# Kernel tuning notes

Measured on AMD Instinct MI355X. Metric: run time of the kernel, lower is better.

The kernel has to match this reference:

```python
import jax, jax.numpy as jnp
import numpy as np

B, T, N, H = 4, 256, 16, 256
NHEAD = 8
FFN = 1024
WIN = 8
EPS = 1e-5


def setup_inputs() -> dict:
    key = jax.random.key(0)
    ks = jax.random.split(key, 10)
    s = 0.02
    return {
        "x": jax.random.normal(ks[0], (B, T, N, H), dtype=jnp.float32),
        "key_padding_mask": jnp.zeros((B, T, N), dtype=bool),
        "Wq": jax.random.normal(ks[1], (H, H), dtype=jnp.float32) * s,
        "bq": jnp.zeros((H,), dtype=jnp.float32),
        "Wk": jax.random.normal(ks[2], (H, H), dtype=jnp.float32) * s,
        "bk": jnp.zeros((H,), dtype=jnp.float32),
        "Wv": jax.random.normal(ks[3], (H, H), dtype=jnp.float32) * s,
        "bv": jnp.zeros((H,), dtype=jnp.float32),
        "W1": jax.random.normal(ks[4], (H, FFN), dtype=jnp.float32) * s,
        "b1": jnp.zeros((FFN,), dtype=jnp.float32),
        "W2": jax.random.normal(ks[5], (FFN, H), dtype=jnp.float32) * s,
        "b2": jnp.zeros((H,), dtype=jnp.float32),
        "g1": jnp.ones((H,), dtype=jnp.float32),
        "beta1": jnp.zeros((H,), dtype=jnp.float32),
        "g2": jnp.ones((H,), dtype=jnp.float32),
        "beta2": jnp.zeros((H,), dtype=jnp.float32),
    }


def _layer_norm(x, g, b):
    m = jnp.mean(x, axis=-1, keepdims=True)
    v = jnp.mean(jnp.square(x - m), axis=-1, keepdims=True)
    return (x - m) * jax.lax.rsqrt(v + EPS) * g + b


def reference(x, key_padding_mask, Wq, bq, Wk, bk, Wv, bv, W1, b1, W2, b2, g1, beta1, g2, beta2):
    Bq, Tq, Nq, Hq = x.shape
    D = Hq // NHEAD
    W = 2 * WIN + 1
    # projections
    q = (x @ Wq + bq).reshape(Bq, Tq, Nq, NHEAD, D) / np.float32(np.sqrt(D))
    k = (x @ Wk + bk).reshape(Bq, Tq, Nq, NHEAD, D)
    v = (x @ Wv + bv).reshape(Bq, Tq, Nq, NHEAD, D)
    idx = jnp.arange(Tq)[:, None] + jnp.arange(W)[None, :] - WIN  # (T, W)
    valid = (idx >= 0) & (idx < Tq)                               # (T, W)
    cidx = jnp.clip(idx, 0, Tq - 1)
    vf6 = valid.reshape(1, Tq, W, 1, 1, 1).astype(q.dtype)
    # gathered window keys/values, zero outside clip: (B, T, W, N, h, D)
    wk = jnp.take(k, cidx, axis=1) * vf6
    wv = jnp.take(v, cidx, axis=1) * vf6
    # attention logits over (W, N) neighbors per head
    logits = jnp.einsum('btnhd,btwmhd->btnwmh', q, wk)  # (B,T,N,W,N,h)
    # mask: padded detections within window, plus out-of-range frames
    kpm_g = jnp.take(key_padding_mask, cidx, axis=1)          # (B,T,W,N)
    mask = jnp.where(valid[None, :, :, None], kpm_g, True)    # (B,T,W,N)
    logits = jnp.where(mask[:, :, None, :, :, None], -jnp.inf, logits)
    attn = jax.nn.softmax(logits.reshape(Bq, Tq, Nq, W * Nq, NHEAD), axis=-2)
    ctx = jnp.einsum('btnmh,btmhd->btnhd', attn,
                     wv.reshape(Bq, Tq, W * Nq, NHEAD, D)).reshape(Bq, Tq, Nq, Hq)
    # residual + LN + FFN + residual + LN (dropout = identity in eval)
    y = _layer_norm(x + ctx, g1, beta1)
    ff = jax.nn.relu(y @ W1 + b1) @ W2 + b2
    return _layer_norm(y + ff, g2, beta2)
```

## Files before the change

kernel.cpp:

```cpp
#include <hip/hip_runtime.h>
#include <hip/hip_bf16.h>
#include <math.h>

typedef __attribute__((ext_vector_type(8))) short short8;
typedef __attribute__((ext_vector_type(4))) float float4v;

#define BB 4
#define TT 256
#define NDET 16
#define HH 256
#define NHEAD 8
#define DD 32
#define FFNDIM 1024
#define ROWS (BB*TT*NDET)
#define EPS 1e-5f

__device__ __forceinline__ unsigned short f2bf(float f) {
  unsigned int u = __float_as_uint(f);
  u += 0x7fffu + ((u >> 16) & 1u);
  return (unsigned short)(u >> 16);
}

__device__ __forceinline__ void wt_tile(const float* __restrict__ W, unsigned short* __restrict__ WT,
                                        int K, int N, int k0, int n0,
                                        float (*tile)[33], int tid) {
  {
    int r = tid >> 3, c4 = (tid & 7) * 4;
    float4 in = *(const float4*)(W + (size_t)(k0 + r) * N + n0 + c4);
    tile[r][c4 + 0] = in.x; tile[r][c4 + 1] = in.y;
    tile[r][c4 + 2] = in.z; tile[r][c4 + 3] = in.w;
  }
  __syncthreads();
  {
    int n = tid >> 3, k4 = (tid & 7) * 4;
    ushort4 o;
    o.x = f2bf(tile[k4 + 0][n]); o.y = f2bf(tile[k4 + 1][n]);
    o.z = f2bf(tile[k4 + 2][n]); o.w = f2bf(tile[k4 + 3][n]);
    *(ushort4*)(WT + (size_t)(n0 + n) * K + k0 + k4) = o;
  }
}

__global__ void prep_kernel(const float* __restrict__ x, const unsigned char* __restrict__ kpm,
                            const float* __restrict__ Wq, const float* __restrict__ Wk,
                            const float* __restrict__ Wv, const float* __restrict__ W1,
                            const float* __restrict__ W2,
                            const float* __restrict__ bq, const float* __restrict__ bk,
                            const float* __restrict__ bv,
                            unsigned short* __restrict__ xb, unsigned short* __restrict__ WqkvT,
                            unsigned short* __restrict__ W1T, unsigned short* __restrict__ W2T,
                            unsigned short* __restrict__ kpm16, float* __restrict__ bqkv) {
  __shared__ float tile[32][33];
  int bid = blockIdx.x, tid = threadIdx.x;
  if (bid < 4096) {
    size_t i = (size_t)(bid * 256 + tid) * 4;
    float4 v = *(const float4*)(x + i);
    ushort4 o = { f2bf(v.x), f2bf(v.y), f2bf(v.z), f2bf(v.w) };
    *(ushort4*)(xb + i) = o;
  } else if (bid < 4288) {
    int t = bid - 4096;
    int wsel = t >> 6, tt = t & 63;
    const float* W = (wsel == 0) ? Wq : (wsel == 1) ? Wk : Wv;
    wt_tile(W, WqkvT + wsel * 65536, 256, 256, (tt >> 3) * 32, (tt & 7) * 32, tile, tid);
  } else if (bid < 4544) {
    int tt = bid - 4288;
    wt_tile(W1, W1T, 256, 1024, (tt >> 5) * 32, (tt & 31) * 32, tile, tid);
  } else if (bid < 4800) {
    int tt = bid - 4544;
    wt_tile(W2, W2T, 1024, 256, (tt >> 3) * 32, (tt & 7) * 32, tile, tid);
  } else if (bid < 4804) {
    int w = (bid - 4800) * 256 + tid;
    uint4 u = *(const uint4*)(kpm + (size_t)w * 16);
    unsigned int a[4] = {u.x, u.y, u.z, u.w};
    unsigned int bits = 0;
#pragma unroll
    for (int m = 0; m < 16; ++m)
      if ((a[m >> 2] >> ((m & 3) * 8)) & 0xffu) bits |= (1u << m);
    kpm16[w] = (unsigned short)bits;
  } else {
    bqkv[tid] = bq[tid];
    bqkv[256 + tid] = bk[tid];
    bqkv[512 + tid] = bv[tid];
  }
}

template<int NROWS, int K>
__device__ __forceinline__ void stage_rows(const unsigned short* __restrict__ src, int kcol0,
                                           char* ldsbase, int tid) {
  constexpr int ISS = NROWS / 32;
  int wave = tid >> 6, lane = tid & 63;
#pragma unroll
  for (int i = 0; i < ISS; ++i) {
    int flat = i * 4096 + wave * 1024 + lane * 16;
    int r = flat >> 7;
    int cb = flat & 127;
    int scb = cb ^ ((r & 7) << 4);
    const unsigned short* g = src + (size_t)r * K + kcol0 + (scb >> 1);
    char* l = ldsbase + i * 4096 + wave * 1024;
    __builtin_amdgcn_global_load_lds((const __attribute__((address_space(1))) void*)g,
                                     (__attribute__((address_space(3))) void*)l, 16, 0, 0);
  }
}

template<int EPI>
__launch_bounds__(256, 2)
__global__ void gemm_kernel(const unsigned short* __restrict__ A,
                            const unsigned short* __restrict__ Bt,
                            const float* __restrict__ bias,
                            unsigned short* __restrict__ q_o, unsigned short* __restrict__ k_o,
                            unsigned short* __restrict__ v_o,
                            unsigned short* __restrict__ outb,
                            const float* __restrict__ yres,
                            const float* __restrict__ gw, const float* __restrict__ bw,
                            float* __restrict__ outf) {
  constexpr int BM = (EPI == 2) ? 64 : 128;
  constexpr int BN = (EPI == 2) ? 256 : 128;
  constexpr int K  = (EPI == 2) ? 1024 : 256;
  constexpr int KP = K / 64;
  constexpr int SMEM = (EPI == 2) ? 67072 : (BM + BN) * 128;
  __shared__ char smem[SMEM];
  const int tid = threadIdx.x;
  const int wave = tid >> 6, lane = tid & 63;
  const int lrow = lane & 15, g = lane >> 4;
  const int m0 = blockIdx.x * BM;
  const int n0 = blockIdx.y * BN;
  const int wr = (EPI == 2) ? 0 : (wave >> 1);
  const int wc = (EPI == 2) ? wave : (wave & 1);
  char* As = smem;
  char* Bs = smem + BM * 128;
  float4v acc[4][4];
#pragma unroll
  for (int i = 0; i < 4; ++i)
#pragma unroll
    for (int j = 0; j < 4; ++j) acc[i][j] = (float4v){0.f, 0.f, 0.f, 0.f};

  const unsigned short* Abase = A + (size_t)m0 * K;
  const unsigned short* Bbase = Bt + (size_t)n0 * K;
  for (int ph = 0; ph < KP; ++ph) {
    if (ph) __syncthreads();
    stage_rows<BM, K>(Abase, ph * 64, As, tid);
    stage_rows<BN, K>(Bbase, ph * 64, Bs, tid);
    __syncthreads();
#pragma unroll
    for (int ks = 0; ks < 2; ++ks) {
      short8 af[4], bf[4];
#pragma unroll
      for (int i = 0; i < 4; ++i) {
        int ar = wr * 64 + i * 16 + lrow;
        af[i] = *(const short8*)(As + ar * 128 + ((ks * 64 + g * 16) ^ ((ar & 7) << 4)));
      }
#pragma unroll
      for (int j = 0; j < 4; ++j) {
        int br = wc * 64 + j * 16 + lrow;
        bf[j] = *(const short8*)(Bs + br * 128 + ((ks * 64 + g * 16) ^ ((br & 7) << 4)));
      }
#pragma unroll
      for (int i = 0; i < 4; ++i)
#pragma unroll
        for (int j = 0; j < 4; ++j)
          acc[i][j] = __builtin_amdgcn_mfma_f32_16x16x32_bf16(af[i], bf[j], acc[i][j], 0, 0, 0);
    }
  }

  if (EPI == 0) {
#pragma unroll
    for (int i = 0; i < 4; ++i)
#pragma unroll
      for (int j = 0; j < 4; ++j) {
        int C = n0 + wc * 64 + j * 16 + lrow;
        float bv = bias[C];
        int proj = C >> 8, cc = C & 255;
        int h = cc >> 5, d = cc & 31;
        unsigned short* om = (proj == 0) ? q_o : ((proj == 1) ? k_o : v_o);
        float sc = (proj == 0) ? 0.17677669529663687f : 1.f;
#pragma unroll
        for (int r = 0; r < 4; ++r) {
          int grow = m0 + wr * 64 + i * 16 + g * 4 + r;
          int b = grow >> 12, tn = grow & 4095;
          om[(size_t)((b * 8 + h) * 4096 + tn) * 32 + d] = f2bf((acc[i][j][r] + bv) * sc);
        }
      }
  } else if (EPI == 1) {
#pragma unroll
    for (int i = 0; i < 4; ++i)
#pragma unroll
      for (int j = 0; j < 4; ++j) {
        int C = n0 + wc * 64 + j * 16 + lrow;
        float bv = bias[C];
#pragma unroll
        for (int r = 0; r < 4; ++r) {
          int grow = m0 + wr * 64 + i * 16 + g * 4 + r;
          outb[(size_t)grow * FFNDIM + C] = f2bf(fmaxf(acc[i][j][r] + bv, 0.f));
        }
      }
  } else {
    __syncthreads();
    float* lnb = (float*)smem;
    float* mrow = (float*)(smem + 64 * 260 * 4);
    float* rrow = mrow + 64;
#pragma unroll
    for (int i = 0; i < 4; ++i)
#pragma unroll
      for (int j = 0; j < 4; ++j) {
        int col = wc * 64 + j * 16 + lrow;
        float bv = bias[col];
#pragma unroll
        for (int r = 0; r < 4; ++r) {
          int ml = i * 16 + g * 4 + r;
          lnb[ml * 260 + col] = acc[i][j][r] + bv + yres[(size_t)(m0 + ml) * 256 + col];
        }
      }
    __syncthreads();
    {
      int row = tid >> 2, part = tid & 3;
      float sm = 0.f;
      for (int ii = 0; ii < 64; ++ii) sm += lnb[row * 260 + part + ii * 4];
      sm += __shfl_xor(sm, 1); sm += __shfl_xor(sm, 2);
      float mean = sm * (1.f / 256.f);
      float vv = 0.f;
      for (int ii = 0; ii < 64; ++ii) {
        float dv = lnb[row * 260 + part + ii * 4] - mean;
        vv += dv * dv;
      }
      vv += __shfl_xor(vv, 1); vv += __shfl_xor(vv, 2);
      if (part == 0) { mrow[row] = mean; rrow[row] = rsqrtf(vv * (1.f / 256.f) + EPS); }
    }
    __syncthreads();
    float gg = gw[tid], bb = bw[tid];
    for (int row = 0; row < 64; ++row) {
      float val = (lnb[row * 260 + tid] - mrow[row]) * rrow[row] * gg + bb;
      outf[(size_t)(m0 + row) * 256 + tid] = val;
    }
  }
}

__global__ void vt_kernel(const unsigned short* __restrict__ v, unsigned short* __restrict__ vT) {
  __shared__ unsigned short tl[64][41];
  int bh = blockIdx.x >> 6, tb = blockIdx.x & 63;
  int tid = threadIdx.x;
  {
    int r = tid >> 2, dp = (tid & 3) * 8;
    short8 in = *(const short8*)(v + ((size_t)bh * 4096 + tb * 64 + r) * 32 + dp);
#pragma unroll
    for (int j = 0; j < 8; ++j) tl[r][dp + j] = (unsigned short)in[j];
  }
  __syncthreads();
  {
    int d = tid >> 3, rp = (tid & 7) * 8;
    short8 ov;
#pragma unroll
    for (int j = 0; j < 8; ++j) ov[j] = (short)tl[rp + j][d];
    *(short8*)(vT + ((size_t)bh * 32 + d) * 4096 + tb * 64 + rp) = ov;
  }
}

__launch_bounds__(64)
__global__ void attn_kernel(const unsigned short* __restrict__ qb,
                            const unsigned short* __restrict__ kb,
                            const unsigned short* __restrict__ vT,
                            const unsigned short* __restrict__ kpm16,
                            float* __restrict__ ctx) {
  __shared__ char P[16 * 640];
  int l = threadIdx.x;
  int idx = blockIdx.x;
  int h = idx & 7, t = (idx >> 3) & 255, b = idx >> 11;
  int lrow = l & 15, g = l >> 4;
  int swz = (lrow & 7) << 4;
#pragma unroll
  for (int i = 0; i < 40; ++i) ((int*)P)[l + i * 64] = 0;
  size_t base = (size_t)(b * 8 + h) * 4096;
  short8 qf = *(const short8*)(qb + (base + t * 16 + lrow) * 32 + g * 8);
  const float4v z4 = {0.f, 0.f, 0.f, 0.f};
  float4v s[17];
#pragma unroll
  for (int w = 0; w < 17; ++w) {
    int j = t + w - 8;
    if (j >= 0 && j < 256) {
      short8 kf = *(const short8*)(kb + (base + j * 16 + lrow) * 32 + g * 8);
      float4v sv = __builtin_amdgcn_mfma_f32_16x16x32_bf16(kf, qf, z4, 0, 0, 0);
      unsigned int mw = kpm16[b * 256 + j];
#pragma unroll
      for (int r = 0; r < 4; ++r)
        if ((mw >> (g * 4 + r)) & 1u) sv[r] = -INFINITY;
      s[w] = sv;
    } else {
      s[w] = (float4v){-INFINITY, -INFINITY, -INFINITY, -INFINITY};
    }
  }
  float mx = -INFINITY;
#pragma unroll
  for (int w = 0; w < 17; ++w)
#pragma unroll
    for (int r = 0; r < 4; ++r) mx = fmaxf(mx, s[w][r]);
  mx = fmaxf(mx, __shfl_xor(mx, 16));
  mx = fmaxf(mx, __shfl_xor(mx, 32));
  float sum = 0.f;
#pragma unroll
  for (int w = 0; w < 17; ++w)
#pragma unroll
    for (int r = 0; r < 4; ++r) {
      float e = __expf(s[w][r] - mx);
      s[w][r] = e; sum += e;
    }
  sum += __shfl_xor(sum, 16);
  sum += __shfl_xor(sum, 32);
  float inv = 1.f / sum;
#pragma unroll
  for (int w = 0; w < 17; ++w) {
#pragma unroll
    for (int r0 = 0; r0 < 4; r0 += 2) {
      unsigned int u = (unsigned int)f2bf(s[w][r0]) | ((unsigned int)f2bf(s[w][r0 + 1]) << 16);
      int kbyte = ((w * 16 + g * 4 + r0) * 2) ^ swz;
      *(int*)(P + lrow * 640 + kbyte) = u;
    }
  }
  __syncthreads();
  float4v o0 = z4, o1 = z4;
  int tn0 = (t - 8) * 16;
  const unsigned short* vbase = vT + ((size_t)(b * 8 + h) * 32 + lrow) * 4096;
#pragma unroll
  for (int c = 0; c < 9; ++c) {
    short8 pf = *(const short8*)(P + lrow * 640 + ((c * 64 + g * 16) ^ swz));
    short8 v0 = *(const short8*)(vbase + tn0 + c * 32 + g * 8);
    short8 v1 = *(const short8*)(vbase + (size_t)16 * 4096 + tn0 + c * 32 + g * 8);
    o0 = __builtin_amdgcn_mfma_f32_16x16x32_bf16(pf, v0, o0, 0, 0, 0);
    o1 = __builtin_amdgcn_mfma_f32_16x16x32_bf16(pf, v1, o1, 0, 0, 0);
  }
  size_t orow = ((size_t)(b * 256 + t)) * 16;
  int col = h * 32 + lrow;
#pragma unroll
  for (int r = 0; r < 4; ++r) {
    float invn = __shfl(inv, g * 4 + r);
    size_t rr = (orow + g * 4 + r) * 256 + col;
    ctx[rr] = o0[r] * invn;
    ctx[rr + 16] = o1[r] * invn;
  }
}

__device__ __forceinline__ float block_sum256(float val, float* sc) {
#pragma unroll
  for (int off = 32; off; off >>= 1) val += __shfl_xor(val, off);
  int wid = threadIdx.x >> 6;
  __syncthreads();
  if ((threadIdx.x & 63) == 0) sc[wid] = val;
  __syncthreads();
  return sc[0] + sc[1] + sc[2] + sc[3];
}

__global__ void ln1_kernel(const float* __restrict__ x, const float* __restrict__ ctxv,
                           const float* __restrict__ gw, const float* __restrict__ bw,
                           float* __restrict__ y, unsigned short* __restrict__ yb) {
  __shared__ float sc[4];
  int row = blockIdx.x, tid = threadIdx.x;
  size_t i = (size_t)row * 256 + tid;
  float val = x[i] + ctxv[i];
  float mean = block_sum256(val, sc) * (1.f / 256.f);
  float dv = val - mean;
  float var = block_sum256(dv * dv, sc) * (1.f / 256.f);
  float o = dv * rsqrtf(var + EPS) * gw[tid] + bw[tid];
  y[i] = o;
  yb[i] = f2bf(o);
}

extern "C" void kernel_launch(void* const* d_in, const int* in_sizes, int n_in,
                              void* d_out, int out_size, void* d_ws, size_t ws_size,
                              hipStream_t stream) {
  const float* x  = (const float*)d_in[0];
  const unsigned char* kpm = (const unsigned char*)d_in[1];
  const float* Wq = (const float*)d_in[2];
  const float* bq = (const float*)d_in[3];
  const float* Wk = (const float*)d_in[4];
  const float* bk = (const float*)d_in[5];
  const float* Wv = (const float*)d_in[6];
  const float* bv = (const float*)d_in[7];
  const float* W1 = (const float*)d_in[8];
  const float* b1 = (const float*)d_in[9];
  const float* W2 = (const float*)d_in[10];
  const float* b2 = (const float*)d_in[11];
  const float* g1 = (const float*)d_in[12];
  const float* be1= (const float*)d_in[13];
  const float* g2 = (const float*)d_in[14];
  const float* be2= (const float*)d_in[15];
  float* out = (float*)d_out;

  char* w = (char*)d_ws;
  const size_t MB = 1u << 20;
  unsigned short* xb   = (unsigned short*)(w);
  unsigned short* qhm  = (unsigned short*)(w + 8 * MB);
  unsigned short* khm  = (unsigned short*)(w + 16 * MB);
  unsigned short* vhm  = (unsigned short*)(w + 24 * MB);
  unsigned short* vTb  = (unsigned short*)(w + 32 * MB);
  float*  ctxv = (float*)(w + 40 * MB);
  float*  yv   = (float*)(w + 56 * MB);
  unsigned short* WqkvT = (unsigned short*)(w + 72 * MB);
  unsigned short* W1T = WqkvT + 196608;
  unsigned short* W2T = W1T + 262144;
  unsigned short* kpm16 = W2T + 262144;
  float* bqkv = (float*)(kpm16 + 1024);
  unsigned short* hid = qhm;
  unsigned short* yb  = xb;

  prep_kernel<<<4805, 256, 0, stream>>>(x, kpm, Wq, Wk, Wv, W1, W2, bq, bk, bv,
                                        xb, WqkvT, W1T, W2T, kpm16, bqkv);
  gemm_kernel<0><<<dim3(128, 6), 256, 0, stream>>>(xb, WqkvT, bqkv, qhm, khm, vhm,
                                                   nullptr, nullptr, nullptr, nullptr, nullptr);
  vt_kernel<<<2048, 256, 0, stream>>>(vhm, vTb);
  attn_kernel<<<8192, 64, 0, stream>>>(qhm, khm, vTb, kpm16, ctxv);
  ln1_kernel<<<16384, 256, 0, stream>>>(x, ctxv, g1, be1, yv, yb);
  gemm_kernel<1><<<dim3(128, 8), 256, 0, stream>>>(yb, W1T, b1, nullptr, nullptr, nullptr,
                                                   hid, nullptr, nullptr, nullptr, nullptr);
  gemm_kernel<2><<<dim3(256, 1), 256, 0, stream>>>(hid, W2T, b2, nullptr, nullptr, nullptr,
                                                   nullptr, yv, g2, be2, out);
}
```

Before: 123.9 us.

## Use bf16 intermediates, 4-head attention blocks, exp2 softmax, new fused FFN2+LN kernel

Several changes land together. The attention context and the LN1 output are now stored as bf16 instead of fp32, and LN1 reads the bf16 copy of x and uses one wave per row with a single-pass mean and variance. Attention packs four heads into each 256-thread block, drops the zeroing of P, uses hardware exp2 with log2e folded into the q scale, and packs bf16 with a single conversion instruction. The FFN2 GEMM with its LayerNorm epilogue moves into a new 512-thread kernel whose row statistics come from register shuffles rather than an LDS pass. Together these cut global memory traffic and instruction count, at the cost of extra bf16 rounding on the residual input and a one-pass variance formula that is less numerically robust.

```diff
diff --git a/kernel.cpp b/kernel.cpp
--- a/kernel.cpp
+++ b/kernel.cpp
@@ -19,6 +19,15 @@
   unsigned int u = __float_as_uint(f);
   u += 0x7fffu + ((u >> 16) & 1u);
   return (unsigned short)(u >> 16);
+}
+__device__ __forceinline__ float bf2f(unsigned short u) {
+  return __uint_as_float((unsigned int)u << 16);
+}
+__device__ __forceinline__ float exp2v(float x) {
+  float r; asm("v_exp_f32 %0, %1" : "=v"(r) : "v"(x)); return r;
+}
+__device__ __forceinline__ unsigned int cvtpk(float lo, float hi) {
+  unsigned int r; asm("v_cvt_pk_bf16_f32 %0, %1, %2" : "=v"(r) : "v"(lo), "v"(hi)); return r;
 }
 
 __device__ __forceinline__ void wt_tile(const float* __restrict__ W, unsigned short* __restrict__ WT,
@@ -83,19 +92,19 @@
   }
 }
 
-template<int NROWS, int K>
+template<int NROWS, int K, int NT>
 __device__ __forceinline__ void stage_rows(const unsigned short* __restrict__ src, int kcol0,
                                            char* ldsbase, int tid) {
-  constexpr int ISS = NROWS / 32;
-  int wave = tid >> 6, lane = tid & 63;
+  constexpr int ISS = NROWS * 8 / NT;
+  int wave = tid >> 6;
 #pragma unroll
   for (int i = 0; i < ISS; ++i) {
-    int flat = i * 4096 + wave * 1024 + lane * 16;
+    int flat = i * (NT * 16) + tid * 16;
     int r = flat >> 7;
     int cb = flat & 127;
     int scb = cb ^ ((r & 7) << 4);
     const unsigned short* g = src + (size_t)r * K + kcol0 + (scb >> 1);
-    char* l = ldsbase + i * 4096 + wave * 1024;
+    char* l = ldsbase + i * (NT * 16) + wave * 1024;
     __builtin_amdgcn_global_load_lds((const __attribute__((address_space(1))) void*)g,
                                      (__attribute__((address_space(3))) void*)l, 16, 0, 0);
   }
@@ -108,23 +117,15 @@
                             const float* __restrict__ bias,
                             unsigned short* __restrict__ q_o, unsigned short* __restrict__ k_o,
                             unsigned short* __restrict__ v_o,
-                            unsigned short* __restrict__ outb,
-                            const float* __restrict__ yres,
-                            const float* __restrict__ gw, const float* __restrict__ bw,
-                            float* __restrict__ outf) {
-  constexpr int BM = (EPI == 2) ? 64 : 128;
-  constexpr int BN = (EPI == 2) ? 256 : 128;
-  constexpr int K  = (EPI == 2) ? 1024 : 256;
-  constexpr int KP = K / 64;
-  constexpr int SMEM = (EPI == 2) ? 67072 : (BM + BN) * 128;
-  __shared__ char smem[SMEM];
+                            unsigned short* __restrict__ outb) {
+  constexpr int BM = 128, BN = 128, K = 256, KP = K / 64;
+  __shared__ char smem[(BM + BN) * 128];
   const int tid = threadIdx.x;
   const int wave = tid >> 6, lane = tid & 63;
   const int lrow = lane & 15, g = lane >> 4;
   const int m0 = blockIdx.x * BM;
   const int n0 = blockIdx.y * BN;
-  const int wr = (EPI == 2) ? 0 : (wave >> 1);
-  const int wc = (EPI == 2) ? wave : (wave & 1);
+  const int wr = wave >> 1, wc = wave & 1;
   char* As = smem;
   char* Bs = smem + BM * 128;
   float4v acc[4][4];
@@ -137,8 +138,8 @@
   const unsigned short* Bbase = Bt + (size_t)n0 * K;
   for (int ph = 0; ph < KP; ++ph) {
     if (ph) __syncthreads();
-    stage_rows<BM, K>(Abase, ph * 64, As, tid);
-    stage_rows<BN, K>(Bbase, ph * 64, Bs, tid);
+    stage_rows<BM, K, 256>(Abase, ph * 64, As, tid);
+    stage_rows<BN, K, 256>(Bbase, ph * 64, Bs, tid);
     __syncthreads();
 #pragma unroll
     for (int ks = 0; ks < 2; ++ks) {
@@ -162,6 +163,7 @@
   }
 
   if (EPI == 0) {
+    const float QS = 0.17677669529663687f * 1.4426950408889634f;
 #pragma unroll
     for (int i = 0; i < 4; ++i)
 #pragma unroll
@@ -171,7 +173,7 @@
         int proj = C >> 8, cc = C & 255;
         int h = cc >> 5, d = cc & 31;
         unsigned short* om = (proj == 0) ? q_o : ((proj == 1) ? k_o : v_o);
-        float sc = (proj == 0) ? 0.17677669529663687f : 1.f;
+        float sc = (proj == 0) ? QS : 1.f;
 #pragma unroll
         for (int r = 0; r < 4; ++r) {
           int grow = m0 + wr * 64 + i * 16 + g * 4 + r;
@@ -179,7 +181,7 @@
           om[(size_t)((b * 8 + h) * 4096 + tn) * 32 + d] = f2bf((acc[i][j][r] + bv) * sc);
         }
       }
-  } else if (EPI == 1) {
+  } else {
 #pragma unroll
     for (int i = 0; i < 4; ++i)
 #pragma unroll
@@ -192,44 +194,6 @@
           outb[(size_t)grow * FFNDIM + C] = f2bf(fmaxf(acc[i][j][r] + bv, 0.f));
         }
       }
-  } else {
-    __syncthreads();
-    float* lnb = (float*)smem;
-    float* mrow = (float*)(smem + 64 * 260 * 4);
-    float* rrow = mrow + 64;
-#pragma unroll
-    for (int i = 0; i < 4; ++i)
-#pragma unroll
-      for (int j = 0; j < 4; ++j) {
-        int col = wc * 64 + j * 16 + lrow;
-        float bv = bias[col];
-#pragma unroll
-        for (int r = 0; r < 4; ++r) {
-          int ml = i * 16 + g * 4 + r;
-          lnb[ml * 260 + col] = acc[i][j][r] + bv + yres[(size_t)(m0 + ml) * 256 + col];
-        }
-      }
-    __syncthreads();
-    {
-      int row = tid >> 2, part = tid & 3;
-      float sm = 0.f;
-      for (int ii = 0; ii < 64; ++ii) sm += lnb[row * 260 + part + ii * 4];
-      sm += __shfl_xor(sm, 1); sm += __shfl_xor(sm, 2);
-      float mean = sm * (1.f / 256.f);
-      float vv = 0.f;
-      for (int ii = 0; ii < 64; ++ii) {
-        float dv = lnb[row * 260 + part + ii * 4] - mean;
-        vv += dv * dv;
-      }
-      vv += __shfl_xor(vv, 1); vv += __shfl_xor(vv, 2);
-      if (part == 0) { mrow[row] = mean; rrow[row] = rsqrtf(vv * (1.f / 256.f) + EPS); }
-    }
-    __syncthreads();
-    float gg = gw[tid], bb = bw[tid];
-    for (int row = 0; row < 64; ++row) {
-      float val = (lnb[row * 260 + tid] - mrow[row]) * rrow[row] * gg + bb;
-      outf[(size_t)(m0 + row) * 256 + tid] = val;
-    }
   }
 }
 
@@ -253,24 +217,26 @@
   }
 }
 
-__launch_bounds__(64)
+__launch_bounds__(256, 4)
 __global__ void attn_kernel(const unsigned short* __restrict__ qb,
                             const unsigned short* __restrict__ kb,
                             const unsigned short* __restrict__ vT,
                             const unsigned short* __restrict__ kpm16,
-                            float* __restrict__ ctx) {
-  __shared__ char P[16 * 640];
-  int l = threadIdx.x;
-  int idx = blockIdx.x;
-  int h = idx & 7, t = (idx >> 3) & 255, b = idx >> 11;
+                            unsigned short* __restrict__ ctxb) {
+  __shared__ char Pall[4][10240];
+  int tid = threadIdx.x;
+  int wave = tid >> 6, l = tid & 63;
+  int bt = blockIdx.x >> 1;
+  int h = (blockIdx.x & 1) * 4 + wave;
+  int t = bt & 255, b = bt >> 8;
+  char* P = Pall[wave];
   int lrow = l & 15, g = l >> 4;
   int swz = (lrow & 7) << 4;
-#pragma unroll
-  for (int i = 0; i < 40; ++i) ((int*)P)[l + i * 64] = 0;
   size_t base = (size_t)(b * 8 + h) * 4096;
   short8 qf = *(const short8*)(qb + (base + t * 16 + lrow) * 32 + g * 8);
   const float4v z4 = {0.f, 0.f, 0.f, 0.f};
   float4v s[17];
+  float mx = -INFINITY;
 #pragma unroll
   for (int w = 0; w < 17; ++w) {
     int j = t + w - 8;
@@ -282,15 +248,12 @@
       for (int r = 0; r < 4; ++r)
         if ((mw >> (g * 4 + r)) & 1u) sv[r] = -INFINITY;
       s[w] = sv;
+#pragma unroll
+      for (int r = 0; r < 4; ++r) mx = fmaxf(mx, sv[r]);
     } else {
       s[w] = (float4v){-INFINITY, -INFINITY, -INFINITY, -INFINITY};
     }
   }
-  float mx = -INFINITY;
-#pragma unroll
-  for (int w = 0; w < 17; ++w)
-#pragma unroll
-    for (int r = 0; r < 4; ++r) mx = fmaxf(mx, s[w][r]);
   mx = fmaxf(mx, __shfl_xor(mx, 16));
   mx = fmaxf(mx, __shfl_xor(mx, 32));
   float sum = 0.f;
@@ -298,7 +261,7 @@
   for (int w = 0; w < 17; ++w)
 #pragma unroll
     for (int r = 0; r < 4; ++r) {
-      float e = __expf(s[w][r] - mx);
+      float e = exp2v(s[w][r] - mx);
       s[w][r] = e; sum += e;
     }
   sum += __shfl_xor(sum, 16);
@@ -306,17 +269,19 @@
   float inv = 1.f / sum;
 #pragma unroll
   for (int w = 0; w < 17; ++w) {
-#pragma unroll
-    for (int r0 = 0; r0 < 4; r0 += 2) {
-      unsigned int u = (unsigned int)f2bf(s[w][r0]) | ((unsigned int)f2bf(s[w][r0 + 1]) << 16);
-      int kbyte = ((w * 16 + g * 4 + r0) * 2) ^ swz;
-      *(int*)(P + lrow * 640 + kbyte) = u;
-    }
-  }
-  __syncthreads();
+    unsigned int u0 = cvtpk(s[w][0], s[w][1]);
+    unsigned int u1 = cvtpk(s[w][2], s[w][3]);
+    *(unsigned int*)(P + lrow * 640 + (((w * 16 + g * 4 + 0) * 2) ^ swz)) = u0;
+    *(unsigned int*)(P + lrow * 640 + (((w * 16 + g * 4 + 2) * 2) ^ swz)) = u1;
+  }
+  *(unsigned int*)(P + lrow * 640 + (((272 + g * 4 + 0) * 2) ^ swz)) = 0u;
+  *(unsigned int*)(P + lrow * 640 + (((272 + g * 4 + 2) * 2) ^ swz)) = 0u;
+  asm volatile("s_waitcnt lgkmcnt(0)" ::: "memory");
+  __builtin_amdgcn_sched_barrier(0);
   float4v o0 = z4, o1 = z4;
   int tn0 = (t - 8) * 16;
   const unsigned short* vbase = vT + ((size_t)(b * 8 + h) * 32 + lrow) * 4096;
+  __builtin_amdgcn_s_setprio(1);
 #pragma unroll
   for (int c = 0; c < 9; ++c) {
     short8 pf = *(const short8*)(P + lrow * 640 + ((c * 64 + g * 16) ^ swz));
@@ -325,40 +290,165 @@
     o0 = __builtin_amdgcn_mfma_f32_16x16x32_bf16(pf, v0, o0, 0, 0, 0);
     o1 = __builtin_amdgcn_mfma_f32_16x16x32_bf16(pf, v1, o1, 0, 0, 0);
   }
+  __builtin_amdgcn_s_setprio(0);
   size_t orow = ((size_t)(b * 256 + t)) * 16;
   int col = h * 32 + lrow;
 #pragma unroll
   for (int r = 0; r < 4; ++r) {
     float invn = __shfl(inv, g * 4 + r);
     size_t rr = (orow + g * 4 + r) * 256 + col;
-    ctx[rr] = o0[r] * invn;
-    ctx[rr + 16] = o1[r] * invn;
-  }
-}
-
-__device__ __forceinline__ float block_sum256(float val, float* sc) {
-#pragma unroll
-  for (int off = 32; off; off >>= 1) val += __shfl_xor(val, off);
-  int wid = threadIdx.x >> 6;
+    ctxb[rr] = f2bf(o0[r] * invn);
+    ctxb[rr + 16] = f2bf(o1[r] * invn);
+  }
+}
+
+__global__ void ln1_kernel(const unsigned short* __restrict__ xb,
+                           const unsigned short* __restrict__ ctxb,
+                           const float* __restrict__ gw, const float* __restrict__ bw,
+                           unsigned short* __restrict__ yb) {
+  int row = blockIdx.x * 4 + (threadIdx.x >> 6);
+  int lane = threadIdx.x & 63;
+  size_t bi = (size_t)row * 256 + lane * 4;
+  ushort4 xv = *(const ushort4*)(xb + bi);
+  ushort4 cv = *(const ushort4*)(ctxb + bi);
+  float v0 = bf2f(xv.x) + bf2f(cv.x);
+  float v1 = bf2f(xv.y) + bf2f(cv.y);
+  float v2 = bf2f(xv.z) + bf2f(cv.z);
+  float v3 = bf2f(xv.w) + bf2f(cv.w);
+  float sm = v0 + v1 + v2 + v3;
+  float sq = v0 * v0 + v1 * v1 + v2 * v2 + v3 * v3;
+#pragma unroll
+  for (int off = 32; off; off >>= 1) {
+    sm += __shfl_xor(sm, off);
+    sq += __shfl_xor(sq, off);
+  }
+  float mean = sm * (1.f / 256.f);
+  float var = sq * (1.f / 256.f) - mean * mean;
+  float rs = rsqrtf(var + EPS);
+  float4 gv = *(const float4*)(gw + lane * 4);
+  float4 bv = *(const float4*)(bw + lane * 4);
+  ushort4 o;
+  o.x = f2bf((v0 - mean) * rs * gv.x + bv.x);
+  o.y = f2bf((v1 - mean) * rs * gv.y + bv.y);
+  o.z = f2bf((v2 - mean) * rs * gv.z + bv.z);
+  o.w = f2bf((v3 - mean) * rs * gv.w + bv.w);
+  *(ushort4*)(yb + bi) = o;
+}
+
+__launch_bounds__(512, 2)
+__global__ void ffn2_kernel(const unsigned short* __restrict__ hid,
+                            const unsigned short* __restrict__ W2T,
+                            const float* __restrict__ b2,
+                            const unsigned short* __restrict__ yb,
+                            const float* __restrict__ gw, const float* __restrict__ bw,
+                            float* __restrict__ out) {
+  constexpr int BM = 64, BN = 256, K = 1024, KP = K / 64;
+  __shared__ char smem[(BM + BN) * 128];
+  __shared__ float stats[8][32][2];
+  __shared__ float mst[64], rst[64];
+  const int tid = threadIdx.x;
+  const int wave = tid >> 6, lane = tid & 63;
+  const int lrow = lane & 15, g = lane >> 4;
+  const int m0 = blockIdx.x * BM;
+  const int wr = wave >> 2, wc = wave & 3;
+  char* As = smem;
+  char* Bs = smem + BM * 128;
+  float4v acc[2][4];
+#pragma unroll
+  for (int i = 0; i < 2; ++i)
+#pragma unroll
+    for (int j = 0; j < 4; ++j) acc[i][j] = (float4v){0.f, 0.f, 0.f, 0.f};
+
+  const unsigned short* Abase = hid + (size_t)m0 * K;
+  for (int ph = 0; ph < KP; ++ph) {
+    if (ph) __syncthreads();
+    stage_rows<BM, K, 512>(Abase, ph * 64, As, tid);
+    stage_rows<BN, K, 512>(W2T, ph * 64, Bs, tid);
+    __syncthreads();
+#pragma unroll
+    for (int ks = 0; ks < 2; ++ks) {
+      short8 af[2], bf[4];
+#pragma unroll
+      for (int i = 0; i < 2; ++i) {
+        int ar = wr * 32 + i * 16 + lrow;
+        af[i] = *(const short8*)(As + ar * 128 + ((ks * 64 + g * 16) ^ ((ar & 7) << 4)));
+      }
+#pragma unroll
+      for (int j = 0; j < 4; ++j) {
+        int br = wc * 64 + j * 16 + lrow;
+        bf[j] = *(const short8*)(Bs + br * 128 + ((ks * 64 + g * 16) ^ ((br & 7) << 4)));
+      }
+#pragma unroll
+      for (int i = 0; i < 2; ++i)
+#pragma unroll
+        for (int j = 0; j < 4; ++j)
+          acc[i][j] = __builtin_amdgcn_mfma_f32_16x16x32_bf16(af[i], bf[j], acc[i][j], 0, 0, 0);
+    }
+  }
   __syncthreads();
-  if ((threadIdx.x & 63) == 0) sc[wid] = val;
+
+#pragma unroll
+  for (int i = 0; i < 2; ++i)
+#pragma unroll
+    for (int j = 0; j < 4; ++j) {
+      int col = wc * 64 + j * 16 + lrow;
+      float bv = b2[col];
+#pragma unroll
+      for (int r = 0; r < 4; ++r) {
+        int row = wr * 32 + i * 16 + g * 4 + r;
+        acc[i][j][r] += bv + bf2f(yb[(size_t)(m0 + row) * 256 + col]);
+      }
+    }
+#pragma unroll
+  for (int i = 0; i < 2; ++i)
+#pragma unroll
+    for (int r = 0; r < 4; ++r) {
+      float sm = acc[i][0][r] + acc[i][1][r] + acc[i][2][r] + acc[i][3][r];
+      float sq = acc[i][0][r] * acc[i][0][r] + acc[i][1][r] * acc[i][1][r]
+               + acc[i][2][r] * acc[i][2][r] + acc[i][3][r] * acc[i][3][r];
+#pragma unroll
+      for (int off = 1; off < 16; off <<= 1) {
+        sm += __shfl_xor(sm, off);
+        sq += __shfl_xor(sq, off);
+      }
+      if (lrow == 0) {
+        stats[wave][i * 16 + g * 4 + r][0] = sm;
+        stats[wave][i * 16 + g * 4 + r][1] = sq;
+      }
+    }
   __syncthreads();
-  return sc[0] + sc[1] + sc[2] + sc[3];
-}
-
-__global__ void ln1_kernel(const float* __restrict__ x, const float* __restrict__ ctxv,
-                           const float* __restrict__ gw, const float* __restrict__ bw,
-                           float* __restrict__ y, unsigned short* __restrict__ yb) {
-  __shared__ float sc[4];
-  int row = blockIdx.x, tid = threadIdx.x;
-  size_t i = (size_t)row * 256 + tid;
-  float val = x[i] + ctxv[i];
-  float mean = block_sum256(val, sc) * (1.f / 256.f);
-  float dv = val - mean;
-  float var = block_sum256(dv * dv, sc) * (1.f / 256.f);
-  float o = dv * rsqrtf(var + EPS) * gw[tid] + bw[tid];
-  y[i] = o;
-  yb[i] = f2bf(o);
+  if (tid < 64) {
+    int wrr = tid >> 5, rl = tid & 31;
+    float S = 0.f, Q = 0.f;
+#pragma unroll
+    for (int w2 = 0; w2 < 4; ++w2) {
+      S += stats[wrr * 4 + w2][rl][0];
+      Q += stats[wrr * 4 + w2][rl][1];
+    }
+    float mean = S * (1.f / 256.f);
+    float var = Q * (1.f / 256.f) - mean * mean;
+    mst[tid] = mean;
+    rst[tid] = rsqrtf(var + EPS);
+  }
+  __syncthreads();
+  float gv[4], bev[4];
+#pragma unroll
+  for (int j = 0; j < 4; ++j) {
+    int col = wc * 64 + j * 16 + lrow;
+    gv[j] = gw[col]; bev[j] = bw[col];
+  }
+#pragma unroll
+  for (int i = 0; i < 2; ++i)
+#pragma unroll
+    for (int r = 0; r < 4; ++r) {
+      int rl = wr * 32 + i * 16 + g * 4 + r;
+      float mean = mst[rl], rs = rst[rl];
+#pragma unroll
+      for (int j = 0; j < 4; ++j) {
+        int col = wc * 64 + j * 16 + lrow;
+        out[(size_t)(m0 + rl) * 256 + col] = (acc[i][j][r] - mean) * rs * gv[j] + bev[j];
+      }
+    }
 }
 
 extern "C" void kernel_launch(void* const* d_in, const int* in_sizes, int n_in,
@@ -389,25 +479,21 @@
   unsigned short* khm  = (unsigned short*)(w + 16 * MB);
   unsigned short* vhm  = (unsigned short*)(w + 24 * MB);
   unsigned short* vTb  = (unsigned short*)(w + 32 * MB);
-  float*  ctxv = (float*)(w + 40 * MB);
-  float*  yv   = (float*)(w + 56 * MB);
+  unsigned short* ctxb = (unsigned short*)(w + 40 * MB);
+  unsigned short* yb   = (unsigned short*)(w + 48 * MB);
   unsigned short* WqkvT = (unsigned short*)(w + 72 * MB);
   unsigned short* W1T = WqkvT + 196608;
   unsigned short* W2T = W1T + 262144;
   unsigned short* kpm16 = W2T + 262144;
   float* bqkv = (float*)(kpm16 + 1024);
   unsigned short* hid = qhm;
-  unsigned short* yb  = xb;
 
   prep_kernel<<<4805, 256, 0, stream>>>(x, kpm, Wq, Wk, Wv, W1, W2, bq, bk, bv,
                                         xb, WqkvT, W1T, W2T, kpm16, bqkv);
-  gemm_kernel<0><<<dim3(128, 6), 256, 0, stream>>>(xb, WqkvT, bqkv, qhm, khm, vhm,
-                                                   nullptr, nullptr, nullptr, nullptr, nullptr);
+  gemm_kernel<0><<<dim3(128, 6), 256, 0, stream>>>(xb, WqkvT, bqkv, qhm, khm, vhm, nullptr);
   vt_kernel<<<2048, 256, 0, stream>>>(vhm, vTb);
-  attn_kernel<<<8192, 64, 0, stream>>>(qhm, khm, vTb, kpm16, ctxv);
-  ln1_kernel<<<16384, 256, 0, stream>>>(x, ctxv, g1, be1, yv, yb);
-  gemm_kernel<1><<<dim3(128, 8), 256, 0, stream>>>(yb, W1T, b1, nullptr, nullptr, nullptr,
-                                                   hid, nullptr, nullptr, nullptr, nullptr);
-  gemm_kernel<2><<<dim3(256, 1), 256, 0, stream>>>(hid, W2T, b2, nullptr, nullptr, nullptr,
-                                                   nullptr, yv, g2, be2, out);
-}
+  attn_kernel<<<2048, 256, 0, stream>>>(qhm, khm, vTb, kpm16, ctxb);
+  ln1_kernel<<<4096, 256, 0, stream>>>(xb, ctxb, g1, be1, yb);
+  gemm_kernel<1><<<dim3(128, 8), 256, 0, stream>>>(yb, W1T, b1, nullptr, nullptr, nullptr, hid);
+  ffn2_kernel<<<256, 512, 0, stream>>>(hid, W2T, b2, yb, g2, be2, out);
+}
```

New measurement: 110.3 us. 1.12x faster.
